# Kernel tuning notes

Hardware: AMD Instinct MI355X
Metric: run time of the kernel (lower is better)

Reference implementation:

```python
import jax, jax.numpy as jnp
import numpy as np

EMBED_DIM = 1024
HIDDEN_DIM = 4096
NUM_EXPERTS = 8
TOP_K = 2


def setup_inputs() -> dict:
    key = jax.random.key(0)
    ks = jax.random.split(key, 5)
    x = jax.random.normal(ks[0], (2, 2048, EMBED_DIM), dtype=jnp.float32)
    Wg = jax.random.normal(ks[1], (EMBED_DIM, NUM_EXPERTS), dtype=jnp.float32) * 0.02
    W1 = jax.random.normal(ks[2], (NUM_EXPERTS, EMBED_DIM, HIDDEN_DIM), dtype=jnp.float32) * 0.02
    W3 = jax.random.normal(ks[3], (NUM_EXPERTS, EMBED_DIM, HIDDEN_DIM), dtype=jnp.float32) * 0.02
    W2 = jax.random.normal(ks[4], (NUM_EXPERTS, HIDDEN_DIM, EMBED_DIM), dtype=jnp.float32) * 0.02
    return {"x": x, "Wg": Wg, "W1": W1, "W3": W3, "W2": W2}


def reference(x, Wg, W1, W3, W2):
    # Gate: linear projection to num_experts logits
    gate = jnp.einsum("bsd,de->bse", x, Wg)  # [B,S,E]
    top_vals, top_idx = jax.lax.top_k(gate, TOP_K)  # [B,S,K]
    sel_w = jax.nn.softmax(top_vals, axis=-1)  # softmax over top-k values
    # Scatter selected weights into dense [B,S,E] (zeros for unselected experts)
    dense_w = jnp.sum(
        jax.nn.one_hot(top_idx, NUM_EXPERTS, dtype=sel_w.dtype) * sel_w[..., None],
        axis=-2,
    )  # [B,S,E]
    # Per-expert SwiGLU FFN; weight=0 for tokens not routed to expert e,
    # so the weighted-sum form is mathematically identical to masked dispatch.
    out = jnp.zeros_like(x)
    for e in range(NUM_EXPERTS):
        h = jax.nn.swish(jnp.einsum("bsd,dh->bsh", x, W1[e])) * jnp.einsum(
            "bsd,dh->bsh", x, W3[e]
        )
        out = out + dense_w[..., e:e + 1] * jnp.einsum("bsh,hd->bsd", h, W2[e])
    return out
```

## Files before the change

kernel.cpp:

```cpp
#include <hip/hip_runtime.h>
#include <hip/hip_bf16.h>
#include <stdint.h>

#define D_EMBED 1024
#define D_HID   4096
#define N_TOK   4096
#define N_EXP   8
#define CAP     4096
#define NROWA   8448

typedef __attribute__((ext_vector_type(4))) float f32x4;
typedef __attribute__((ext_vector_type(8))) short bf16x8;

__device__ __forceinline__ unsigned short f2bf(float f) {
    unsigned int u = __builtin_bit_cast(unsigned int, f);
    u += 0x7fffu + ((u >> 16) & 1u);
    return (unsigned short)(u >> 16);
}

__device__ __forceinline__ void gload_lds16(const void* g, void* l) {
    __builtin_amdgcn_global_load_lds(
        (const __attribute__((address_space(1))) unsigned int*)g,
        (__attribute__((address_space(3))) unsigned int*)l,
        16, 0, 0);
}

__global__ __launch_bounds__(256) void pack_w(const float* __restrict__ W,
                                              unsigned short* __restrict__ out, int R, int C) {
    int e = blockIdx.z, kb = blockIdx.y, cb = blockIdx.x;
    const float* Wp = W + (size_t)e * R * C + (size_t)(kb * 64) * C + cb * 64;
    unsigned short* op = out + (size_t)e * R * C;
    __shared__ unsigned short lds[64][72];
    int t = threadIdx.x;
    int r = t >> 2;
    int c0 = (t & 3) << 4;
    const float* src = Wp + (size_t)r * C + c0;
#pragma unroll
    for (int i = 0; i < 2; ++i) {
        f32x4 a = *reinterpret_cast<const f32x4*>(src + i * 8);
        f32x4 b = *reinterpret_cast<const f32x4*>(src + i * 8 + 4);
        bf16x8 o;
        o[0]=(short)f2bf(a[0]); o[1]=(short)f2bf(a[1]); o[2]=(short)f2bf(a[2]); o[3]=(short)f2bf(a[3]);
        o[4]=(short)f2bf(b[0]); o[5]=(short)f2bf(b[1]); o[6]=(short)f2bf(b[2]); o[7]=(short)f2bf(b[3]);
        *reinterpret_cast<bf16x8*>(&lds[r][c0 + i * 8]) = o;
    }
    __syncthreads();
#pragma unroll
    for (int i = 0; i < 2; ++i) {
        int cell = i * 256 + t;
        int ksl = cell >> 6, col = cell & 63;
        bf16x8 o;
#pragma unroll
        for (int j = 0; j < 8; ++j) o[j] = (short)lds[ksl * 8 + j][col];
        *reinterpret_cast<bf16x8*>(op + ((size_t)(kb * 8 + ksl) * C + cb * 64 + col) * 8) = o;
    }
}

__global__ __launch_bounds__(256) void pack_w13(const float* __restrict__ W1,
                                                const float* __restrict__ W3,
                                                unsigned short* __restrict__ out) {
    int e = blockIdx.z, kb = blockIdx.y, cb = blockIdx.x;
    size_t ebase = (size_t)e * D_EMBED * D_HID;
    const float* b1 = W1 + ebase + (size_t)(kb * 64) * D_HID + cb * 32;
    const float* b3 = W3 + ebase + (size_t)(kb * 64) * D_HID + cb * 32;
    unsigned short* op = out + (size_t)e * D_EMBED * 2 * D_HID;
    __shared__ unsigned short lds[64][72];
    int t = threadIdx.x;
    int r = t >> 2, ck = t & 3;
    const float* src = (ck >= 2 ? b3 : b1) + (size_t)r * D_HID + (ck & 1) * 16;
#pragma unroll
    for (int i = 0; i < 2; ++i) {
        f32x4 a = *reinterpret_cast<const f32x4*>(src + i * 8);
        f32x4 b = *reinterpret_cast<const f32x4*>(src + i * 8 + 4);
        bf16x8 o;
        o[0]=(short)f2bf(a[0]); o[1]=(short)f2bf(a[1]); o[2]=(short)f2bf(a[2]); o[3]=(short)f2bf(a[3]);
        o[4]=(short)f2bf(b[0]); o[5]=(short)f2bf(b[1]); o[6]=(short)f2bf(b[2]); o[7]=(short)f2bf(b[3]);
        *reinterpret_cast<bf16x8*>(&lds[r][ck * 16 + i * 8]) = o;
    }
    __syncthreads();
#pragma unroll
    for (int i = 0; i < 2; ++i) {
        int cell = i * 256 + t;
        int ksl = cell >> 6, pcp = cell & 63;
        int lcol = ((pcp >> 4) & 1) * 32 + ((pcp >> 5) & 1) * 16 + (pcp & 15);
        bf16x8 o;
#pragma unroll
        for (int j = 0; j < 8; ++j) o[j] = (short)lds[ksl * 8 + j][lcol];
        *reinterpret_cast<bf16x8*>(op + ((size_t)(kb * 8 + ksl) * (2 * D_HID) + cb * 64 + pcp) * 8) = o;
    }
}

__global__ __launch_bounds__(256) void gate_kernel(const float* __restrict__ x,
                                                   const float* __restrict__ Wg,
                                                   int* __restrict__ counts,
                                                   int* __restrict__ toks,
                                                   float* __restrict__ wgts,
                                                   int* __restrict__ slots) {
    int wave = threadIdx.x >> 6;
    int lane = threadIdx.x & 63;
    int tok = blockIdx.x * 4 + wave;
    const float* xp = x + (size_t)tok * D_EMBED;
    float acc[8] = {0, 0, 0, 0, 0, 0, 0, 0};
#pragma unroll
    for (int i = 0; i < 16; ++i) {
        int d = lane + 64 * i;
        float xv = xp[d];
        f32x4 w0 = *reinterpret_cast<const f32x4*>(Wg + (size_t)d * 8);
        f32x4 w1 = *reinterpret_cast<const f32x4*>(Wg + (size_t)d * 8 + 4);
        acc[0] += xv * w0[0]; acc[1] += xv * w0[1]; acc[2] += xv * w0[2]; acc[3] += xv * w0[3];
        acc[4] += xv * w1[0]; acc[5] += xv * w1[1]; acc[6] += xv * w1[2]; acc[7] += xv * w1[3];
    }
#pragma unroll
    for (int e = 0; e < 8; ++e)
        for (int s = 32; s; s >>= 1) acc[e] += __shfl_xor(acc[e], s, 64);
    if (lane == 0) {
        int i0 = 0; float v0 = acc[0];
#pragma unroll
        for (int e = 1; e < 8; ++e) if (acc[e] > v0) { v0 = acc[e]; i0 = e; }
        int i1 = -1; float v1 = -1e30f;
#pragma unroll
        for (int e = 0; e < 8; ++e) if (e != i0 && acc[e] > v1) { v1 = acc[e]; i1 = e; }
        float ex = __expf(v1 - v0);
        float w0 = 1.0f / (1.0f + ex);
        float w1 = 1.0f - w0;
        int p0 = atomicAdd(&counts[i0], 1);
        toks[i0 * CAP + p0] = tok; wgts[i0 * CAP + p0] = w0; slots[i0 * CAP + p0] = 0;
        int p1 = atomicAdd(&counts[i1], 1);
        toks[i1 * CAP + p1] = tok; wgts[i1 * CAP + p1] = w1; slots[i1 * CAP + p1] = 1;
    }
}

__global__ void prefix_kernel(const int* __restrict__ counts, int* __restrict__ offsets) {
    if (threadIdx.x == 0) {
        int s = 0;
        for (int e = 0; e < N_EXP; ++e) { offsets[e] = s; s += counts[e]; }
    }
}

__global__ __launch_bounds__(256) void build_map_kernel(const int* __restrict__ counts,
                                                        const int* __restrict__ offsets,
                                                        const int* __restrict__ toks,
                                                        const int* __restrict__ slots,
                                                        int* __restrict__ tok2row) {
    int i = blockIdx.x * 256 + threadIdx.x;
    int e = i >> 12, pos = i & (CAP - 1);
    if (pos < counts[e])
        tok2row[toks[i] * 2 + slots[i]] = offsets[e] + pos;
}

__global__ __launch_bounds__(256) void gather_x_kernel(
    const float* __restrict__ x,
    const int* __restrict__ counts, const int* __restrict__ offsets,
    const int* __restrict__ toks,
    unsigned short* __restrict__ xg) {
    int rt = blockIdx.x;
    int e = -1, base = 0, rowbase = 0, cnt = 0;
    for (int ee = 0; ee < N_EXP; ++ee) {
        int c = counts[ee];
        int nt = (c + 63) >> 6;
        if (rt < base + nt) { e = ee; rowbase = (rt - base) << 6; cnt = c; break; }
        base += nt;
    }
    if (e < 0) return;
    int off = offsets[e];
    int kb = blockIdx.y;
    __shared__ unsigned short lds[64][72];
    int t = threadIdx.x;
    int r = t >> 2, ck = t & 3;
    int pos = rowbase + r;
    unsigned short tmp[16];
    if (pos < cnt) {
        int tok = toks[e * CAP + pos];
        const float* src = x + (size_t)tok * D_EMBED + kb * 64 + ck * 16;
#pragma unroll
        for (int i = 0; i < 4; ++i) {
            f32x4 v = *reinterpret_cast<const f32x4*>(src + i * 4);
#pragma unroll
            for (int j = 0; j < 4; ++j) tmp[i * 4 + j] = f2bf(v[j]);
        }
    } else {
#pragma unroll
        for (int i = 0; i < 16; ++i) tmp[i] = 0;
    }
#pragma unroll
    for (int i = 0; i < 16; ++i) lds[r][ck * 16 + i] = tmp[i];
    __syncthreads();
    int sl = t >> 5, rr = (t & 31) * 2;
#pragma unroll
    for (int w = 0; w < 2; ++w) {
        int rw = rr + w;
        if (rowbase + rw >= cnt) continue;
        bf16x8 o;
#pragma unroll
        for (int j = 0; j < 8; ++j) o[j] = (short)lds[rw][sl * 8 + j];
        *reinterpret_cast<bf16x8*>(xg + ((size_t)(kb * 8 + sl) * NROWA + off + rowbase + rw) * 8) = o;
    }
}

__global__ __launch_bounds__(512, 1) void gemm1_kernel(
    const unsigned short* __restrict__ xg,
    const unsigned short* __restrict__ wt13,
    const int* __restrict__ counts, const int* __restrict__ offsets,
    const float* __restrict__ wgts,
    unsigned short* __restrict__ hp) {
    int rt = blockIdx.y;
    int e = -1, base = 0, rowbase = 0, cnt = 0;
#pragma unroll 1
    for (int ee = 0; ee < N_EXP; ++ee) {
        int c = counts[ee];
        int nt = (c + 255) >> 8;
        if (rt < base + nt) { e = ee; rowbase = (rt - base) << 8; cnt = c; break; }
        base += nt;
    }
    if (e < 0) return;
    int off = offsets[e];
    int colp = blockIdx.x * 256;

    __shared__ __align__(16) char lds[4][32768];

    int t = threadIdx.x, lane = t & 63, w = t >> 6;
    int wr = w >> 2, wc = w & 3;
    int q = lane >> 4, p = lane & 15;

    const unsigned short* wB = wt13 + (size_t)e * D_EMBED * 2 * D_HID;
    const unsigned short* pA = xg + (size_t)(off + rowbase) * 8;

    f32x4 acc[8][4] = {};

    auto STG = [&](int h, int j) {
        char* L = &lds[h & 3][0];
        int flat = j * 512 + t;
        size_t gs = (size_t)(h * 4 + (flat >> 8));
        int rc = flat & 255;
        gload_lds16(pA + (gs * NROWA + rc) * 8, L + flat * 16);
        gload_lds16(wB + (gs * (2 * D_HID) + colp + rc) * 8, L + 16384 + flat * 16);
    };

    STG(0, 0); STG(0, 1); STG(1, 0); STG(1, 1);
    asm volatile("s_waitcnt vmcnt(4)" ::: "memory");
    __builtin_amdgcn_s_barrier();
    asm volatile("" ::: "memory");

#pragma unroll 1
    for (int h = 0; h < 32; ++h) {
        const char* L = &lds[h & 3][0];
        if (h < 30) STG(h + 2, 0);
        bf16x8 af[8], bf[4];
#pragma unroll
        for (int m = 0; m < 8; ++m)
            af[m] = *reinterpret_cast<const bf16x8*>(L + (q * 256 + wr * 128 + m * 16 + p) * 16);
#pragma unroll
        for (int n = 0; n < 4; ++n)
            bf[n] = *reinterpret_cast<const bf16x8*>(L + 16384 + (q * 256 + wc * 64 + n * 16 + p) * 16);
        asm volatile("" ::: "memory");
        __builtin_amdgcn_s_barrier();
        __builtin_amdgcn_s_setprio(1);
#pragma unroll
        for (int n = 0; n < 2; ++n)
#pragma unroll
            for (int m = 0; m < 8; ++m)
                acc[m][n] = __builtin_amdgcn_mfma_f32_16x16x32_bf16(af[m], bf[n], acc[m][n], 0, 0, 0);
        __builtin_amdgcn_s_setprio(0);
        asm volatile("" ::: "memory");
        if (h < 30) asm volatile("s_waitcnt vmcnt(2)" ::: "memory");
        else        asm volatile("s_waitcnt vmcnt(0)" ::: "memory");
        if (h < 30) STG(h + 2, 1);
        asm volatile("" ::: "memory");
        __builtin_amdgcn_s_barrier();
        __builtin_amdgcn_s_setprio(1);
#pragma unroll
        for (int n = 2; n < 4; ++n)
#pragma unroll
            for (int m = 0; m < 8; ++m)
                acc[m][n] = __builtin_amdgcn_mfma_f32_16x16x32_bf16(af[m], bf[n], acc[m][n], 0, 0, 0);
        __builtin_amdgcn_s_setprio(0);
        asm volatile("" ::: "memory");
    }

#pragma unroll
    for (int m = 0; m < 8; ++m) {
#pragma unroll
        for (int reg = 0; reg < 4; ++reg) {
            int rl = wr * 128 + m * 16 + q * 4 + reg;
            int grow = rowbase + rl;
            if (grow >= cnt) continue;
            float wgt = wgts[e * CAP + grow];
            size_t row = (size_t)(off + grow);
#pragma unroll
            for (int np = 0; np < 2; ++np) {
                float a1 = acc[m][2 * np][reg];
                float a3 = acc[m][2 * np + 1][reg];
                float hv = (a1 / (1.0f + __expf(-a1))) * a3 * wgt;
                int rc = (blockIdx.x * 8 + wc * 2 + np) * 16 + p;
                hp[((size_t)(rc >> 3) * NROWA + row) * 8 + (rc & 7)] = f2bf(hv);
            }
        }
    }
}

__global__ __launch_bounds__(512, 1) void gemm2_kernel(
    const unsigned short* __restrict__ hp,
    const unsigned short* __restrict__ wt2,
    const int* __restrict__ counts, const int* __restrict__ offsets,
    float* __restrict__ pbuf) {
    int rt = blockIdx.y;
    int e = -1, base = 0, rowbase = 0, cnt = 0;
#pragma unroll 1
    for (int ee = 0; ee < N_EXP; ++ee) {
        int c = counts[ee];
        int nt = (c + 255) >> 8;
        if (rt < base + nt) { e = ee; rowbase = (rt - base) << 8; cnt = c; break; }
        base += nt;
    }
    if (e < 0) return;
    int off = offsets[e];
    int colb = blockIdx.x * 256;
    int s2 = blockIdx.z;

    __shared__ __align__(16) char lds[4][32768];

    int t = threadIdx.x, lane = t & 63, w = t >> 6;
    int wr = w >> 2, wc = w & 3;
    int q = lane >> 4, p = lane & 15;

    const unsigned short* wB = wt2 + (size_t)e * D_HID * D_EMBED;
    const unsigned short* pA = hp + (size_t)(off + rowbase) * 8;

    f32x4 acc[8][4] = {};

    auto STG = [&](int h, int j) {
        char* L = &lds[h & 3][0];
        int flat = j * 512 + t;
        size_t gs = (size_t)(s2 * 128 + h * 4 + (flat >> 8));
        int rc = flat & 255;
        gload_lds16(pA + (gs * NROWA + rc) * 8, L + flat * 16);
        gload_lds16(wB + (gs * D_EMBED + colb + rc) * 8, L + 16384 + flat * 16);
    };

    STG(0, 0); STG(0, 1); STG(1, 0); STG(1, 1);
    asm volatile("s_waitcnt vmcnt(4)" ::: "memory");
    __builtin_amdgcn_s_barrier();
    asm volatile("" ::: "memory");

#pragma unroll 1
    for (int h = 0; h < 32; ++h) {
        const char* L = &lds[h & 3][0];
        if (h < 30) STG(h + 2, 0);
        bf16x8 af[8], bf[4];
#pragma unroll
        for (int m = 0; m < 8; ++m)
            af[m] = *reinterpret_cast<const bf16x8*>(L + (q * 256 + wr * 128 + m * 16 + p) * 16);
#pragma unroll
        for (int n = 0; n < 4; ++n)
            bf[n] = *reinterpret_cast<const bf16x8*>(L + 16384 + (q * 256 + wc * 64 + n * 16 + p) * 16);
        asm volatile("" ::: "memory");
        __builtin_amdgcn_s_barrier();
        __builtin_amdgcn_s_setprio(1);
#pragma unroll
        for (int n = 0; n < 2; ++n)
#pragma unroll
            for (int m = 0; m < 8; ++m)
                acc[m][n] = __builtin_amdgcn_mfma_f32_16x16x32_bf16(af[m], bf[n], acc[m][n], 0, 0, 0);
        __builtin_amdgcn_s_setprio(0);
        asm volatile("" ::: "memory");
        if (h < 30) asm volatile("s_waitcnt vmcnt(2)" ::: "memory");
        else        asm volatile("s_waitcnt vmcnt(0)" ::: "memory");
        if (h < 30) STG(h + 2, 1);
        asm volatile("" ::: "memory");
        __builtin_amdgcn_s_barrier();
        __builtin_amdgcn_s_setprio(1);
#pragma unroll
        for (int n = 2; n < 4; ++n)
#pragma unroll
            for (int m = 0; m < 8; ++m)
                acc[m][n] = __builtin_amdgcn_mfma_f32_16x16x32_bf16(af[m], bf[n], acc[m][n], 0, 0, 0);
        __builtin_amdgcn_s_setprio(0);
        asm volatile("" ::: "memory");
    }

    float* pb = pbuf + (size_t)s2 * 8192 * D_EMBED;
#pragma unroll
    for (int m = 0; m < 8; ++m)
#pragma unroll
        for (int reg = 0; reg < 4; ++reg) {
            int rl = wr * 128 + m * 16 + q * 4 + reg;
            int grow = rowbase + rl;
            if (grow >= cnt) continue;
            float* dst = pb + (size_t)(off + grow) * D_EMBED + colb + wc * 64;
#pragma unroll
            for (int n = 0; n < 4; ++n) dst[n * 16 + p] = acc[m][n][reg];
        }
}

__global__ __launch_bounds__(256) void combine_kernel(const float* __restrict__ pbuf,
                                                      const int* __restrict__ tok2row,
                                                      float* __restrict__ out) {
    int i = blockIdx.x * 256 + threadIdx.x;
    int tok = i >> 8, c = (i & 255) * 4;
    int r0 = tok2row[tok * 2], r1 = tok2row[tok * 2 + 1];
    const size_t SP = (size_t)8192 * D_EMBED;
    f32x4 s = {0.f, 0.f, 0.f, 0.f};
#pragma unroll
    for (int sp = 0; sp < 4; ++sp) {
        f32x4 a = *reinterpret_cast<const f32x4*>(pbuf + sp * SP + (size_t)r0 * D_EMBED + c);
        f32x4 b = *reinterpret_cast<const f32x4*>(pbuf + sp * SP + (size_t)r1 * D_EMBED + c);
        s = s + a + b;
    }
    *reinterpret_cast<f32x4*>(out + (size_t)tok * D_EMBED + c) = s;
}

extern "C" void kernel_launch(void* const* d_in, const int* in_sizes, int n_in,
                              void* d_out, int out_size, void* d_ws, size_t ws_size,
                              hipStream_t stream) {
    const float* x  = (const float*)d_in[0];
    const float* Wg = (const float*)d_in[1];
    const float* W1 = (const float*)d_in[2];
    const float* W3 = (const float*)d_in[3];
    const float* W2 = (const float*)d_in[4];
    float* out = (float*)d_out;

    char* ws = (char*)d_ws;
    size_t szW = (size_t)N_EXP * D_EMBED * D_HID;
    unsigned short* wt13 = (unsigned short*)ws; ws += szW * 2 * 2;
    unsigned short* wt2  = (unsigned short*)ws; ws += szW * 2;
    unsigned short* hp   = (unsigned short*)ws; ws += (size_t)(D_HID / 8) * NROWA * 8 * 2;
    unsigned short* xg   = (unsigned short*)ws; ws += (size_t)(D_EMBED / 8) * NROWA * 8 * 2;
    int*   toks    = (int*)ws;   ws += (size_t)N_EXP * CAP * 4;
    float* wgts    = (float*)ws; ws += (size_t)N_EXP * CAP * 4;
    int*   slots   = (int*)ws;   ws += (size_t)N_EXP * CAP * 4;
    int*   tok2row = (int*)ws;   ws += (size_t)N_TOK * 2 * 4;
    int*   counts  = (int*)ws;   ws += 8 * 4;
    int*   offsets = (int*)ws;   ws += 8 * 4;
    float* pbuf = (float*)wt13;

    hipMemsetAsync(counts, 0, 8 * sizeof(int), stream);

    pack_w13<<<dim3(128, 16, N_EXP), 256, 0, stream>>>(W1, W3, wt13);
    pack_w<<<dim3(D_EMBED / 64, D_HID / 64, N_EXP), 256, 0, stream>>>(W2, wt2, D_HID, D_EMBED);
    gate_kernel<<<N_TOK / 4, 256, 0, stream>>>(x, Wg, counts, toks, wgts, slots);
    prefix_kernel<<<1, 64, 0, stream>>>(counts, offsets);
    build_map_kernel<<<(N_EXP * CAP) / 256, 256, 0, stream>>>(counts, offsets, toks, slots, tok2row);
    gather_x_kernel<<<dim3(136, D_EMBED / 64), 256, 0, stream>>>(x, counts, offsets, toks, xg);
    gemm1_kernel<<<dim3(32, 39), 512, 0, stream>>>(xg, wt13, counts, offsets, wgts, hp);
    gemm2_kernel<<<dim3(4, 39, 4), 512, 0, stream>>>(hp, wt2, counts, offsets, pbuf);
    combine_kernel<<<(N_TOK * 256) / 256, 256, 0, stream>>>(pbuf, tok2row, out);
}
```

Baseline: 542.4 us.

## Shrink GEMM row tiles to 128, triple-buffer LDS, bf16 partials, simpler packing

Both expert GEMMs move from 256-row to 128-row tiles. This gives more blocks (72 row tiles instead of 39) and lets four blocks share a CU, using a 3-slot LDS ring with pointer-stepped global-to-LDS loads. The weight-packing kernels become direct strided per-thread transposes with no LDS staging. The prefix kernel is removed and offsets are computed inline from the counts. GEMM2 partial sums are now stored as bf16 instead of fp32 to halve pbuf traffic in combine, which costs some accuracy in the split-K reduction.

Result: faster. 475.1 us (-12.4%).

```diff
diff --git a/kernel.cpp b/kernel.cpp
--- a/kernel.cpp
+++ b/kernel.cpp
@@ -17,77 +17,42 @@
     u += 0x7fffu + ((u >> 16) & 1u);
     return (unsigned short)(u >> 16);
 }
-
+__device__ __forceinline__ float bf2f(unsigned short h) {
+    unsigned int u = ((unsigned int)h) << 16;
+    return __builtin_bit_cast(float, u);
+}
 __device__ __forceinline__ void gload_lds16(const void* g, void* l) {
     __builtin_amdgcn_global_load_lds(
         (const __attribute__((address_space(1))) unsigned int*)g,
-        (__attribute__((address_space(3))) unsigned int*)l,
-        16, 0, 0);
-}
-
-__global__ __launch_bounds__(256) void pack_w(const float* __restrict__ W,
-                                              unsigned short* __restrict__ out, int R, int C) {
-    int e = blockIdx.z, kb = blockIdx.y, cb = blockIdx.x;
-    const float* Wp = W + (size_t)e * R * C + (size_t)(kb * 64) * C + cb * 64;
-    unsigned short* op = out + (size_t)e * R * C;
-    __shared__ unsigned short lds[64][72];
-    int t = threadIdx.x;
-    int r = t >> 2;
-    int c0 = (t & 3) << 4;
-    const float* src = Wp + (size_t)r * C + c0;
-#pragma unroll
-    for (int i = 0; i < 2; ++i) {
-        f32x4 a = *reinterpret_cast<const f32x4*>(src + i * 8);
-        f32x4 b = *reinterpret_cast<const f32x4*>(src + i * 8 + 4);
-        bf16x8 o;
-        o[0]=(short)f2bf(a[0]); o[1]=(short)f2bf(a[1]); o[2]=(short)f2bf(a[2]); o[3]=(short)f2bf(a[3]);
-        o[4]=(short)f2bf(b[0]); o[5]=(short)f2bf(b[1]); o[6]=(short)f2bf(b[2]); o[7]=(short)f2bf(b[3]);
-        *reinterpret_cast<bf16x8*>(&lds[r][c0 + i * 8]) = o;
-    }
-    __syncthreads();
-#pragma unroll
-    for (int i = 0; i < 2; ++i) {
-        int cell = i * 256 + t;
-        int ksl = cell >> 6, col = cell & 63;
-        bf16x8 o;
-#pragma unroll
-        for (int j = 0; j < 8; ++j) o[j] = (short)lds[ksl * 8 + j][col];
-        *reinterpret_cast<bf16x8*>(op + ((size_t)(kb * 8 + ksl) * C + cb * 64 + col) * 8) = o;
-    }
+        (__attribute__((address_space(3))) unsigned int*)l, 16, 0, 0);
 }
 
 __global__ __launch_bounds__(256) void pack_w13(const float* __restrict__ W1,
                                                 const float* __restrict__ W3,
                                                 unsigned short* __restrict__ out) {
-    int e = blockIdx.z, kb = blockIdx.y, cb = blockIdx.x;
-    size_t ebase = (size_t)e * D_EMBED * D_HID;
-    const float* b1 = W1 + ebase + (size_t)(kb * 64) * D_HID + cb * 32;
-    const float* b3 = W3 + ebase + (size_t)(kb * 64) * D_HID + cb * 32;
-    unsigned short* op = out + (size_t)e * D_EMBED * 2 * D_HID;
-    __shared__ unsigned short lds[64][72];
-    int t = threadIdx.x;
-    int r = t >> 2, ck = t & 3;
-    const float* src = (ck >= 2 ? b3 : b1) + (size_t)r * D_HID + (ck & 1) * 16;
-#pragma unroll
-    for (int i = 0; i < 2; ++i) {
-        f32x4 a = *reinterpret_cast<const f32x4*>(src + i * 8);
-        f32x4 b = *reinterpret_cast<const f32x4*>(src + i * 8 + 4);
-        bf16x8 o;
-        o[0]=(short)f2bf(a[0]); o[1]=(short)f2bf(a[1]); o[2]=(short)f2bf(a[2]); o[3]=(short)f2bf(a[3]);
-        o[4]=(short)f2bf(b[0]); o[5]=(short)f2bf(b[1]); o[6]=(short)f2bf(b[2]); o[7]=(short)f2bf(b[3]);
-        *reinterpret_cast<bf16x8*>(&lds[r][ck * 16 + i * 8]) = o;
-    }
-    __syncthreads();
-#pragma unroll
-    for (int i = 0; i < 2; ++i) {
-        int cell = i * 256 + t;
-        int ksl = cell >> 6, pcp = cell & 63;
-        int lcol = ((pcp >> 4) & 1) * 32 + ((pcp >> 5) & 1) * 16 + (pcp & 15);
-        bf16x8 o;
-#pragma unroll
-        for (int j = 0; j < 8; ++j) o[j] = (short)lds[ksl * 8 + j][lcol];
-        *reinterpret_cast<bf16x8*>(op + ((size_t)(kb * 8 + ksl) * (2 * D_HID) + cb * 64 + pcp) * 8) = o;
-    }
+    int idx = blockIdx.x * 256 + threadIdx.x;
+    int pc = idx & 8191, s = (idx >> 13) & 127, e = idx >> 20;
+    int g = pc >> 4;
+    int rc = ((g >> 1) << 4) + (pc & 15);
+    const float* src = (g & 1 ? W3 : W1) + (size_t)e * (D_EMBED * D_HID)
+                     + (size_t)(s * 8) * D_HID + rc;
+    bf16x8 o;
+#pragma unroll
+    for (int j = 0; j < 8; ++j) o[j] = (short)f2bf(src[(size_t)j * D_HID]);
+    *reinterpret_cast<bf16x8*>(out + (size_t)e * (D_EMBED * 2 * D_HID)
+                               + ((size_t)s * (2 * D_HID) + pc) * 8) = o;
+}
+
+__global__ __launch_bounds__(256) void pack_w(const float* __restrict__ W,
+                                              unsigned short* __restrict__ out) {
+    int idx = blockIdx.x * 256 + threadIdx.x;
+    int col = idx & 1023, s = (idx >> 10) & 511, e = idx >> 19;
+    const float* src = W + (size_t)e * (D_HID * D_EMBED) + (size_t)(s * 8) * D_EMBED + col;
+    bf16x8 o;
+#pragma unroll
+    for (int j = 0; j < 8; ++j) o[j] = (short)f2bf(src[(size_t)j * D_EMBED]);
+    *reinterpret_cast<bf16x8*>(out + (size_t)e * (D_HID * D_EMBED)
+                               + ((size_t)s * D_EMBED + col) * 8) = o;
 }
 
 __global__ __launch_bounds__(256) void gate_kernel(const float* __restrict__ x,
@@ -130,39 +95,30 @@
     }
 }
 
-__global__ void prefix_kernel(const int* __restrict__ counts, int* __restrict__ offsets) {
-    if (threadIdx.x == 0) {
-        int s = 0;
-        for (int e = 0; e < N_EXP; ++e) { offsets[e] = s; s += counts[e]; }
-    }
-}
-
 __global__ __launch_bounds__(256) void build_map_kernel(const int* __restrict__ counts,
-                                                        const int* __restrict__ offsets,
                                                         const int* __restrict__ toks,
                                                         const int* __restrict__ slots,
                                                         int* __restrict__ tok2row) {
     int i = blockIdx.x * 256 + threadIdx.x;
     int e = i >> 12, pos = i & (CAP - 1);
-    if (pos < counts[e])
-        tok2row[toks[i] * 2 + slots[i]] = offsets[e] + pos;
+    if (pos >= counts[e]) return;
+    int off = 0;
+    for (int k = 0; k < e; ++k) off += counts[k];
+    tok2row[toks[i] * 2 + slots[i]] = off + pos;
 }
 
 __global__ __launch_bounds__(256) void gather_x_kernel(
-    const float* __restrict__ x,
-    const int* __restrict__ counts, const int* __restrict__ offsets,
-    const int* __restrict__ toks,
-    unsigned short* __restrict__ xg) {
+    const float* __restrict__ x, const int* __restrict__ counts,
+    const int* __restrict__ toks, unsigned short* __restrict__ xg) {
     int rt = blockIdx.x;
-    int e = -1, base = 0, rowbase = 0, cnt = 0;
+    int e = -1, tb = 0, osum = 0, rowbase = 0, cnt = 0, off = 0;
     for (int ee = 0; ee < N_EXP; ++ee) {
         int c = counts[ee];
         int nt = (c + 63) >> 6;
-        if (rt < base + nt) { e = ee; rowbase = (rt - base) << 6; cnt = c; break; }
-        base += nt;
+        if (rt < tb + nt) { e = ee; rowbase = (rt - tb) << 6; cnt = c; off = osum; break; }
+        tb += nt; osum += c;
     }
     if (e < 0) return;
-    int off = offsets[e];
     int kb = blockIdx.y;
     __shared__ unsigned short lds[64][72];
     int t = threadIdx.x;
@@ -197,91 +153,94 @@
     }
 }
 
-__global__ __launch_bounds__(512, 1) void gemm1_kernel(
+__global__ __launch_bounds__(512, 4) void gemm1_kernel(
     const unsigned short* __restrict__ xg,
     const unsigned short* __restrict__ wt13,
-    const int* __restrict__ counts, const int* __restrict__ offsets,
+    const int* __restrict__ counts,
     const float* __restrict__ wgts,
     unsigned short* __restrict__ hp) {
     int rt = blockIdx.y;
-    int e = -1, base = 0, rowbase = 0, cnt = 0;
+    int e = -1, tb = 0, osum = 0, rowbase = 0, cnt = 0, off = 0;
 #pragma unroll 1
     for (int ee = 0; ee < N_EXP; ++ee) {
         int c = counts[ee];
-        int nt = (c + 255) >> 8;
-        if (rt < base + nt) { e = ee; rowbase = (rt - base) << 8; cnt = c; break; }
-        base += nt;
+        int nt = (c + 127) >> 7;
+        if (rt < tb + nt) { e = ee; rowbase = (rt - tb) << 7; cnt = c; off = osum; break; }
+        tb += nt; osum += c;
     }
     if (e < 0) return;
-    int off = offsets[e];
     int colp = blockIdx.x * 256;
 
-    __shared__ __align__(16) char lds[4][32768];
+    __shared__ __align__(16) char lds[3][24576];
 
     int t = threadIdx.x, lane = t & 63, w = t >> 6;
     int wr = w >> 2, wc = w & 3;
     int q = lane >> 4, p = lane & 15;
 
-    const unsigned short* wB = wt13 + (size_t)e * D_EMBED * 2 * D_HID;
-    const unsigned short* pA = xg + (size_t)(off + rowbase) * 8;
-
-    f32x4 acc[8][4] = {};
-
-    auto STG = [&](int h, int j) {
-        char* L = &lds[h & 3][0];
-        int flat = j * 512 + t;
-        size_t gs = (size_t)(h * 4 + (flat >> 8));
-        int rc = flat & 255;
-        gload_lds16(pA + (gs * NROWA + rc) * 8, L + flat * 16);
-        gload_lds16(wB + (gs * (2 * D_HID) + colp + rc) * 8, L + 16384 + flat * 16);
+    const size_t ASTEP = (size_t)4 * NROWA * 16;
+    const size_t BSTEP = (size_t)4 * (2 * D_HID) * 16;
+    const char* aS = (const char*)xg + ((size_t)(t >> 7) * NROWA + off + rowbase + (t & 127)) * 16;
+    const char* bS0 = (const char*)wt13 + (size_t)e * D_EMBED * 2 * D_HID * 2
+                    + ((size_t)(t >> 8) * (2 * D_HID) + colp + (t & 255)) * 16;
+    const char* bS1 = bS0 + (size_t)2 * (2 * D_HID) * 16;
+
+    int wslot = 0;
+    auto STG = [&]() {
+        char* L = &lds[wslot][0];
+        wslot = (wslot == 2) ? 0 : wslot + 1;
+        gload_lds16(aS, L + t * 16);                 aS += ASTEP;
+        gload_lds16(bS0, L + 8192 + t * 16);         bS0 += BSTEP;
+        gload_lds16(bS1, L + 16384 + t * 16);        bS1 += BSTEP;
     };
 
-    STG(0, 0); STG(0, 1); STG(1, 0); STG(1, 1);
-    asm volatile("s_waitcnt vmcnt(4)" ::: "memory");
+    f32x4 acc[4][4] = {};
+
+    STG(); STG();
+    asm volatile("s_waitcnt vmcnt(3)" ::: "memory");
     __builtin_amdgcn_s_barrier();
     asm volatile("" ::: "memory");
 
+    int rslot = 0;
 #pragma unroll 1
     for (int h = 0; h < 32; ++h) {
-        const char* L = &lds[h & 3][0];
-        if (h < 30) STG(h + 2, 0);
-        bf16x8 af[8], bf[4];
-#pragma unroll
-        for (int m = 0; m < 8; ++m)
-            af[m] = *reinterpret_cast<const bf16x8*>(L + (q * 256 + wr * 128 + m * 16 + p) * 16);
+        const char* L = &lds[rslot][0];
+        rslot = (rslot == 2) ? 0 : rslot + 1;
+        if (h < 30) STG();
+        bf16x8 af[4], bf[4];
+#pragma unroll
+        for (int m = 0; m < 4; ++m)
+            af[m] = *reinterpret_cast<const bf16x8*>(L + (q * 128 + wr * 64 + m * 16 + p) * 16);
 #pragma unroll
         for (int n = 0; n < 4; ++n)
-            bf[n] = *reinterpret_cast<const bf16x8*>(L + 16384 + (q * 256 + wc * 64 + n * 16 + p) * 16);
+            bf[n] = *reinterpret_cast<const bf16x8*>(L + 8192 + (q * 256 + wc * 64 + n * 16 + p) * 16);
         asm volatile("" ::: "memory");
         __builtin_amdgcn_s_barrier();
         __builtin_amdgcn_s_setprio(1);
 #pragma unroll
         for (int n = 0; n < 2; ++n)
 #pragma unroll
-            for (int m = 0; m < 8; ++m)
+            for (int m = 0; m < 4; ++m)
                 acc[m][n] = __builtin_amdgcn_mfma_f32_16x16x32_bf16(af[m], bf[n], acc[m][n], 0, 0, 0);
         __builtin_amdgcn_s_setprio(0);
         asm volatile("" ::: "memory");
-        if (h < 30) asm volatile("s_waitcnt vmcnt(2)" ::: "memory");
+        if (h < 30) asm volatile("s_waitcnt vmcnt(3)" ::: "memory");
         else        asm volatile("s_waitcnt vmcnt(0)" ::: "memory");
-        if (h < 30) STG(h + 2, 1);
-        asm volatile("" ::: "memory");
         __builtin_amdgcn_s_barrier();
         __builtin_amdgcn_s_setprio(1);
 #pragma unroll
         for (int n = 2; n < 4; ++n)
 #pragma unroll
-            for (int m = 0; m < 8; ++m)
+            for (int m = 0; m < 4; ++m)
                 acc[m][n] = __builtin_amdgcn_mfma_f32_16x16x32_bf16(af[m], bf[n], acc[m][n], 0, 0, 0);
         __builtin_amdgcn_s_setprio(0);
         asm volatile("" ::: "memory");
     }
 
 #pragma unroll
-    for (int m = 0; m < 8; ++m) {
+    for (int m = 0; m < 4; ++m) {
 #pragma unroll
         for (int reg = 0; reg < 4; ++reg) {
-            int rl = wr * 128 + m * 16 + q * 4 + reg;
+            int rl = wr * 64 + m * 16 + q * 4 + reg;
             int grow = rowbase + rl;
             if (grow >= cnt) continue;
             float wgt = wgts[e * CAP + grow];
@@ -298,115 +257,124 @@
     }
 }
 
-__global__ __launch_bounds__(512, 1) void gemm2_kernel(
+__global__ __launch_bounds__(512, 4) void gemm2_kernel(
     const unsigned short* __restrict__ hp,
     const unsigned short* __restrict__ wt2,
-    const int* __restrict__ counts, const int* __restrict__ offsets,
-    float* __restrict__ pbuf) {
+    const int* __restrict__ counts,
+    unsigned short* __restrict__ pbuf) {
     int rt = blockIdx.y;
-    int e = -1, base = 0, rowbase = 0, cnt = 0;
+    int e = -1, tb = 0, osum = 0, rowbase = 0, cnt = 0, off = 0;
 #pragma unroll 1
     for (int ee = 0; ee < N_EXP; ++ee) {
         int c = counts[ee];
-        int nt = (c + 255) >> 8;
-        if (rt < base + nt) { e = ee; rowbase = (rt - base) << 8; cnt = c; break; }
-        base += nt;
+        int nt = (c + 127) >> 7;
+        if (rt < tb + nt) { e = ee; rowbase = (rt - tb) << 7; cnt = c; off = osum; break; }
+        tb += nt; osum += c;
     }
     if (e < 0) return;
-    int off = offsets[e];
     int colb = blockIdx.x * 256;
     int s2 = blockIdx.z;
 
-    __shared__ __align__(16) char lds[4][32768];
+    __shared__ __align__(16) char lds[3][24576];
 
     int t = threadIdx.x, lane = t & 63, w = t >> 6;
     int wr = w >> 2, wc = w & 3;
     int q = lane >> 4, p = lane & 15;
 
-    const unsigned short* wB = wt2 + (size_t)e * D_HID * D_EMBED;
-    const unsigned short* pA = hp + (size_t)(off + rowbase) * 8;
-
-    f32x4 acc[8][4] = {};
-
-    auto STG = [&](int h, int j) {
-        char* L = &lds[h & 3][0];
-        int flat = j * 512 + t;
-        size_t gs = (size_t)(s2 * 128 + h * 4 + (flat >> 8));
-        int rc = flat & 255;
-        gload_lds16(pA + (gs * NROWA + rc) * 8, L + flat * 16);
-        gload_lds16(wB + (gs * D_EMBED + colb + rc) * 8, L + 16384 + flat * 16);
+    const size_t ASTEP = (size_t)4 * NROWA * 16;
+    const size_t BSTEP = (size_t)4 * D_EMBED * 16;
+    const char* aS = (const char*)hp
+        + ((size_t)(s2 * 128 + (t >> 7)) * NROWA + off + rowbase + (t & 127)) * 16;
+    const char* bS0 = (const char*)wt2 + (size_t)e * D_HID * D_EMBED * 2
+        + ((size_t)(s2 * 128 + (t >> 8)) * D_EMBED + colb + (t & 255)) * 16;
+    const char* bS1 = bS0 + (size_t)2 * D_EMBED * 16;
+
+    int wslot = 0;
+    auto STG = [&]() {
+        char* L = &lds[wslot][0];
+        wslot = (wslot == 2) ? 0 : wslot + 1;
+        gload_lds16(aS, L + t * 16);                 aS += ASTEP;
+        gload_lds16(bS0, L + 8192 + t * 16);         bS0 += BSTEP;
+        gload_lds16(bS1, L + 16384 + t * 16);        bS1 += BSTEP;
     };
 
-    STG(0, 0); STG(0, 1); STG(1, 0); STG(1, 1);
-    asm volatile("s_waitcnt vmcnt(4)" ::: "memory");
+    f32x4 acc[4][4] = {};
+
+    STG(); STG();
+    asm volatile("s_waitcnt vmcnt(3)" ::: "memory");
     __builtin_amdgcn_s_barrier();
     asm volatile("" ::: "memory");
 
+    int rslot = 0;
 #pragma unroll 1
     for (int h = 0; h < 32; ++h) {
-        const char* L = &lds[h & 3][0];
-        if (h < 30) STG(h + 2, 0);
-        bf16x8 af[8], bf[4];
-#pragma unroll
-        for (int m = 0; m < 8; ++m)
-            af[m] = *reinterpret_cast<const bf16x8*>(L + (q * 256 + wr * 128 + m * 16 + p) * 16);
+        const char* L = &lds[rslot][0];
+        rslot = (rslot == 2) ? 0 : rslot + 1;
+        if (h < 30) STG();
+        bf16x8 af[4], bf[4];
+#pragma unroll
+        for (int m = 0; m < 4; ++m)
+            af[m] = *reinterpret_cast<const bf16x8*>(L + (q * 128 + wr * 64 + m * 16 + p) * 16);
 #pragma unroll
         for (int n = 0; n < 4; ++n)
-            bf[n] = *reinterpret_cast<const bf16x8*>(L + 16384 + (q * 256 + wc * 64 + n * 16 + p) * 16);
+            bf[n] = *reinterpret_cast<const bf16x8*>(L + 8192 + (q * 256 + wc * 64 + n * 16 + p) * 16);
         asm volatile("" ::: "memory");
         __builtin_amdgcn_s_barrier();
         __builtin_amdgcn_s_setprio(1);
 #pragma unroll
         for (int n = 0; n < 2; ++n)
 #pragma unroll
-            for (int m = 0; m < 8; ++m)
+            for (int m = 0; m < 4; ++m)
                 acc[m][n] = __builtin_amdgcn_mfma_f32_16x16x32_bf16(af[m], bf[n], acc[m][n], 0, 0, 0);
         __builtin_amdgcn_s_setprio(0);
         asm volatile("" ::: "memory");
-        if (h < 30) asm volatile("s_waitcnt vmcnt(2)" ::: "memory");
+        if (h < 30) asm volatile("s_waitcnt vmcnt(3)" ::: "memory");
         else        asm volatile("s_waitcnt vmcnt(0)" ::: "memory");
-        if (h < 30) STG(h + 2, 1);
-        asm volatile("" ::: "memory");
         __builtin_amdgcn_s_barrier();
         __builtin_amdgcn_s_setprio(1);
 #pragma unroll
         for (int n = 2; n < 4; ++n)
 #pragma unroll
-            for (int m = 0; m < 8; ++m)
+            for (int m = 0; m < 4; ++m)
                 acc[m][n] = __builtin_amdgcn_mfma_f32_16x16x32_bf16(af[m], bf[n], acc[m][n], 0, 0, 0);
         __builtin_amdgcn_s_setprio(0);
         asm volatile("" ::: "memory");
     }
 
-    float* pb = pbuf + (size_t)s2 * 8192 * D_EMBED;
-#pragma unroll
-    for (int m = 0; m < 8; ++m)
+    unsigned short* pb = pbuf + (size_t)s2 * 8192 * D_EMBED;
+#pragma unroll
+    for (int m = 0; m < 4; ++m)
 #pragma unroll
         for (int reg = 0; reg < 4; ++reg) {
-            int rl = wr * 128 + m * 16 + q * 4 + reg;
+            int rl = wr * 64 + m * 16 + q * 4 + reg;
             int grow = rowbase + rl;
             if (grow >= cnt) continue;
-            float* dst = pb + (size_t)(off + grow) * D_EMBED + colb + wc * 64;
-#pragma unroll
-            for (int n = 0; n < 4; ++n) dst[n * 16 + p] = acc[m][n][reg];
+            unsigned short* dst = pb + (size_t)(off + grow) * D_EMBED + colb + wc * 64;
+#pragma unroll
+            for (int n = 0; n < 4; ++n) dst[n * 16 + p] = f2bf(acc[m][n][reg]);
         }
 }
 
-__global__ __launch_bounds__(256) void combine_kernel(const float* __restrict__ pbuf,
+__global__ __launch_bounds__(256) void combine_kernel(const unsigned short* __restrict__ pbuf,
                                                       const int* __restrict__ tok2row,
                                                       float* __restrict__ out) {
     int i = blockIdx.x * 256 + threadIdx.x;
-    int tok = i >> 8, c = (i & 255) * 4;
+    int tok = i >> 7, c0 = (i & 127) * 8;
     int r0 = tok2row[tok * 2], r1 = tok2row[tok * 2 + 1];
     const size_t SP = (size_t)8192 * D_EMBED;
-    f32x4 s = {0.f, 0.f, 0.f, 0.f};
+    float s[8] = {0, 0, 0, 0, 0, 0, 0, 0};
 #pragma unroll
     for (int sp = 0; sp < 4; ++sp) {
-        f32x4 a = *reinterpret_cast<const f32x4*>(pbuf + sp * SP + (size_t)r0 * D_EMBED + c);
-        f32x4 b = *reinterpret_cast<const f32x4*>(pbuf + sp * SP + (size_t)r1 * D_EMBED + c);
-        s = s + a + b;
-    }
-    *reinterpret_cast<f32x4*>(out + (size_t)tok * D_EMBED + c) = s;
+        bf16x8 a = *reinterpret_cast<const bf16x8*>(pbuf + sp * SP + (size_t)r0 * D_EMBED + c0);
+        bf16x8 b = *reinterpret_cast<const bf16x8*>(pbuf + sp * SP + (size_t)r1 * D_EMBED + c0);
+#pragma unroll
+        for (int j = 0; j < 8; ++j)
+            s[j] += bf2f((unsigned short)a[j]) + bf2f((unsigned short)b[j]);
+    }
+    float* op = out + (size_t)tok * D_EMBED + c0;
+    f32x4 lo = {s[0], s[1], s[2], s[3]}, hi = {s[4], s[5], s[6], s[7]};
+    *reinterpret_cast<f32x4*>(op) = lo;
+    *reinterpret_cast<f32x4*>(op + 4) = hi;
 }
 
 extern "C" void kernel_launch(void* const* d_in, const int* in_sizes, int n_in,
@@ -430,18 +398,16 @@
     int*   slots   = (int*)ws;   ws += (size_t)N_EXP * CAP * 4;
     int*   tok2row = (int*)ws;   ws += (size_t)N_TOK * 2 * 4;
     int*   counts  = (int*)ws;   ws += 8 * 4;
-    int*   offsets = (int*)ws;   ws += 8 * 4;
-    float* pbuf = (float*)wt13;
+    unsigned short* pbuf = (unsigned short*)wt13;
 
     hipMemsetAsync(counts, 0, 8 * sizeof(int), stream);
 
-    pack_w13<<<dim3(128, 16, N_EXP), 256, 0, stream>>>(W1, W3, wt13);
-    pack_w<<<dim3(D_EMBED / 64, D_HID / 64, N_EXP), 256, 0, stream>>>(W2, wt2, D_HID, D_EMBED);
+    pack_w13<<<32768, 256, 0, stream>>>(W1, W3, wt13);
+    pack_w<<<16384, 256, 0, stream>>>(W2, wt2);
     gate_kernel<<<N_TOK / 4, 256, 0, stream>>>(x, Wg, counts, toks, wgts, slots);
-    prefix_kernel<<<1, 64, 0, stream>>>(counts, offsets);
-    build_map_kernel<<<(N_EXP * CAP) / 256, 256, 0, stream>>>(counts, offsets, toks, slots, tok2row);
-    gather_x_kernel<<<dim3(136, D_EMBED / 64), 256, 0, stream>>>(x, counts, offsets, toks, xg);
-    gemm1_kernel<<<dim3(32, 39), 512, 0, stream>>>(xg, wt13, counts, offsets, wgts, hp);
-    gemm2_kernel<<<dim3(4, 39, 4), 512, 0, stream>>>(hp, wt2, counts, offsets, pbuf);
-    combine_kernel<<<(N_TOK * 256) / 256, 256, 0, stream>>>(pbuf, tok2row, out);
-}
+    build_map_kernel<<<(N_EXP * CAP) / 256, 256, 0, stream>>>(counts, toks, slots, tok2row);
+    gather_x_kernel<<<dim3(136, D_EMBED / 64), 256, 0, stream>>>(x, counts, toks, xg);
+    gemm1_kernel<<<dim3(32, 72), 512, 0, stream>>>(xg, wt13, counts, wgts, hp);
+    gemm2_kernel<<<dim3(4, 72, 4), 512, 0, stream>>>(hp, wt2, counts, pbuf);
+    combine_kernel<<<(N_TOK * 128) / 256, 256, 0, stream>>>(pbuf, tok2row, out);
+}
```
